# Performance work log

Measured on AMD Instinct MI355X. Metric: run time of the kernel, lower is better.

## Reference

```python
import jax, jax.numpy as jnp
import numpy as np

IN_FEATURES = 4096
OUT_FEATURES = 4096
BATCH = 16384


def setup_inputs() -> dict:
    key = jax.random.key(0)
    k_x, k_w, k_b = jax.random.split(key, 3)
    x = jax.random.normal(k_x, (BATCH, IN_FEATURES), dtype=jnp.float32)
    # nn.Linear default init: U(-1/sqrt(in), 1/sqrt(in))
    bound = 1.0 / np.sqrt(IN_FEATURES)
    W = jax.random.uniform(k_w, (OUT_FEATURES, IN_FEATURES), dtype=jnp.float32,
                           minval=-bound, maxval=bound)
    bias = jax.random.uniform(k_b, (OUT_FEATURES,), dtype=jnp.float32,
                              minval=-bound, maxval=bound)
    return {"x": x, "W": W, "bias": bias}


def reference(x, W, bias):
    # Algebraic reduction: sum_j (x @ W.T + b)[i, j]
    #   = x @ sum_j W[j, :] + sum_j b[j]
    weight_sums = jnp.sum(W, axis=0)          # [in_features]
    bias_sum = jnp.sum(bias)                  # scalar
    out = x @ weight_sums + bias_sum          # [batch]
    return out[:, None]                       # [batch, 1]
```

## Files before the change

### kernel.cpp

```cpp
#include <hip/hip_runtime.h>

#define IN_F 4096
#define OUT_F 4096
#define BATCH 16384


__global__ __launch_bounds__(256) void colsum_kernel(
    const float* __restrict__ W, const float* __restrict__ bias,
    float* __restrict__ ws) {
  const int ROWS_PER_CHUNK = OUT_F / 64;
  int col4 = blockIdx.x * 256 + threadIdx.x;
  int row0 = blockIdx.y * ROWS_PER_CHUNK;
  const float4* W4 = (const float4*)W;

  float4 acc = make_float4(0.f, 0.f, 0.f, 0.f);
  #pragma unroll 8
  for (int r = 0; r < ROWS_PER_CHUNK; ++r) {
    float4 v = W4[(size_t)(row0 + r) * (IN_F / 4) + col4];
    acc.x += v.x; acc.y += v.y; acc.z += v.z; acc.w += v.w;
  }
  atomicAdd(&ws[col4 * 4 + 0], acc.x);
  atomicAdd(&ws[col4 * 4 + 1], acc.y);
  atomicAdd(&ws[col4 * 4 + 2], acc.z);
  atomicAdd(&ws[col4 * 4 + 3], acc.w);

  if (blockIdx.x == 0 && blockIdx.y == 0) {
    float b = 0.f;
    for (int i = threadIdx.x; i < OUT_F; i += 256) b += bias[i];
    #pragma unroll
    for (int off = 32; off > 0; off >>= 1) b += __shfl_down(b, off);
    if ((threadIdx.x & 63) == 0) atomicAdd(&ws[IN_F], b);
  }
}

__global__ __launch_bounds__(256) void rowdot_kernel(
    const float* __restrict__ x, const float* __restrict__ ws,
    float* __restrict__ out) {
  __shared__ float4 sw[IN_F / 4];
  __shared__ float sbias;

  const float4* ws4 = (const float4*)ws;
  for (int i = threadIdx.x; i < IN_F / 4; i += 256) sw[i] = ws4[i];
  if (threadIdx.x == 0) sbias = ws[IN_F];
  __syncthreads();

  int wave = threadIdx.x >> 6;
  int lane = threadIdx.x & 63;
  int row  = blockIdx.x * 4 + wave;

  const float4* xr = (const float4*)(x + (size_t)row * IN_F);
  float acc = 0.f;
  #pragma unroll
  for (int it = 0; it < IN_F / 4 / 64; ++it) {
    float4 xv = xr[it * 64 + lane];
    float4 wv = sw[it * 64 + lane];
    acc += xv.x * wv.x + xv.y * wv.y + xv.z * wv.z + xv.w * wv.w;
  }
  #pragma unroll
  for (int off = 32; off > 0; off >>= 1) acc += __shfl_down(acc, off);
  if (lane == 0) out[row] = acc + sbias;
}

extern "C" void kernel_launch(void* const* d_in, const int* in_sizes, int n_in,
                              void* d_out, int out_size, void* d_ws, size_t ws_size,
                              hipStream_t stream) {
  const float* x    = (const float*)d_in[0];
  const float* W    = (const float*)d_in[1];
  const float* bias = (const float*)d_in[2];
  float* out = (float*)d_out;
  float* ws  = (float*)d_ws;

  hipMemsetAsync(ws, 0, (IN_F + 1) * sizeof(float), stream);

  dim3 g1(4, 64);
  colsum_kernel<<<g1, 256, 0, stream>>>(W, bias, ws);

  rowdot_kernel<<<BATCH / 4, 256, 0, stream>>>(x, ws, out);
}
```

Measured before the change: 401.7 us.

## Replace atomic column-sum and memset with two-pass partial reduction; drop LDS staging

Column sums of W are now written as per-chunk partials and then reduced by a separate small kernel, which removes the float atomics and the memset launch. The bias sum moves into the reduce kernel. The rowdot kernel no longer stages the weight-sum vector in shared memory and instead reads it straight from global memory, relying on the cache, which also removes a __syncthreads. This trades one memset for an extra kernel launch plus a 1 MB partial buffer write and read.

```diff
diff --git a/kernel.cpp b/kernel.cpp
--- a/kernel.cpp
+++ b/kernel.cpp
@@ -4,11 +4,14 @@
 #define OUT_F 4096
 #define BATCH 16384
 
+#define NCHUNK 64
+#define ROWS_PER_CHUNK (OUT_F / NCHUNK)
+#define PART_F4 (IN_F / 4)
+#define CS_OFF   (NCHUNK * IN_F)
+#define BIAS_OFF (CS_OFF + IN_F)
 
-__global__ __launch_bounds__(256) void colsum_kernel(
-    const float* __restrict__ W, const float* __restrict__ bias,
-    float* __restrict__ ws) {
-  const int ROWS_PER_CHUNK = OUT_F / 64;
+__global__ __launch_bounds__(256) void colsum_part(
+    const float* __restrict__ W, float* __restrict__ ws) {
   int col4 = blockIdx.x * 256 + threadIdx.x;
   int row0 = blockIdx.y * ROWS_PER_CHUNK;
   const float4* W4 = (const float4*)W;
@@ -16,49 +19,54 @@
   float4 acc = make_float4(0.f, 0.f, 0.f, 0.f);
   #pragma unroll 8
   for (int r = 0; r < ROWS_PER_CHUNK; ++r) {
-    float4 v = W4[(size_t)(row0 + r) * (IN_F / 4) + col4];
+    float4 v = W4[(size_t)(row0 + r) * PART_F4 + col4];
     acc.x += v.x; acc.y += v.y; acc.z += v.z; acc.w += v.w;
   }
-  atomicAdd(&ws[col4 * 4 + 0], acc.x);
-  atomicAdd(&ws[col4 * 4 + 1], acc.y);
-  atomicAdd(&ws[col4 * 4 + 2], acc.z);
-  atomicAdd(&ws[col4 * 4 + 3], acc.w);
+  ((float4*)ws)[(size_t)blockIdx.y * PART_F4 + col4] = acc;
+}
 
-  if (blockIdx.x == 0 && blockIdx.y == 0) {
+__global__ __launch_bounds__(256) void colsum_reduce(
+    const float* __restrict__ bias, float* __restrict__ ws) {
+  if (blockIdx.x < 4) {
+    int col4 = blockIdx.x * 256 + threadIdx.x;
+    const float4* p4 = (const float4*)ws;
+    float4 acc = make_float4(0.f, 0.f, 0.f, 0.f);
+    #pragma unroll 8
+    for (int k = 0; k < NCHUNK; ++k) {
+      float4 v = p4[(size_t)k * PART_F4 + col4];
+      acc.x += v.x; acc.y += v.y; acc.z += v.z; acc.w += v.w;
+    }
+    ((float4*)(ws + CS_OFF))[col4] = acc;
+  } else if (threadIdx.x < 64) {
     float b = 0.f;
-    for (int i = threadIdx.x; i < OUT_F; i += 256) b += bias[i];
+    #pragma unroll
+    for (int i = 0; i < OUT_F / 64; ++i) b += bias[threadIdx.x + i * 64];
     #pragma unroll
     for (int off = 32; off > 0; off >>= 1) b += __shfl_down(b, off);
-    if ((threadIdx.x & 63) == 0) atomicAdd(&ws[IN_F], b);
+    if (threadIdx.x == 0) ws[BIAS_OFF] = b;
   }
 }
 
 __global__ __launch_bounds__(256) void rowdot_kernel(
     const float* __restrict__ x, const float* __restrict__ ws,
     float* __restrict__ out) {
-  __shared__ float4 sw[IN_F / 4];
-  __shared__ float sbias;
-
-  const float4* ws4 = (const float4*)ws;
-  for (int i = threadIdx.x; i < IN_F / 4; i += 256) sw[i] = ws4[i];
-  if (threadIdx.x == 0) sbias = ws[IN_F];
-  __syncthreads();
-
   int wave = threadIdx.x >> 6;
   int lane = threadIdx.x & 63;
   int row  = blockIdx.x * 4 + wave;
 
-  const float4* xr = (const float4*)(x + (size_t)row * IN_F);
+  const float4* xr  = (const float4*)(x + (size_t)row * IN_F);
+  const float4* cs4 = (const float4*)(ws + CS_OFF);
+
   float acc = 0.f;
   #pragma unroll
   for (int it = 0; it < IN_F / 4 / 64; ++it) {
     float4 xv = xr[it * 64 + lane];
-    float4 wv = sw[it * 64 + lane];
+    float4 wv = cs4[it * 64 + lane];
     acc += xv.x * wv.x + xv.y * wv.y + xv.z * wv.z + xv.w * wv.w;
   }
   #pragma unroll
   for (int off = 32; off > 0; off >>= 1) acc += __shfl_down(acc, off);
-  if (lane == 0) out[row] = acc + sbias;
+  if (lane == 0) out[row] = acc + ws[BIAS_OFF];
 }
 
 extern "C" void kernel_launch(void* const* d_in, const int* in_sizes, int n_in,
@@ -70,10 +78,7 @@
   float* out = (float*)d_out;
   float* ws  = (float*)d_ws;
 
-  hipMemsetAsync(ws, 0, (IN_F + 1) * sizeof(float), stream);
-
-  dim3 g1(4, 64);
-  colsum_kernel<<<g1, 256, 0, stream>>>(W, bias, ws);
-
+  colsum_part<<<dim3(4, NCHUNK), 256, 0, stream>>>(W, ws);
+  colsum_reduce<<<5, 256, 0, stream>>>(bias, ws);
   rowdot_kernel<<<BATCH / 4, 256, 0, stream>>>(x, ws, out);
 }
```

Measured after the change: 395.9 us. About the same (-1.5%).
